# Performance work log

Hardware: AMD Instinct MI355X
Metric: run time of the kernel (lower is better)

## Reference

```python
import jax, jax.numpy as jnp
import numpy as np

DIM = 384
EPS = 1e-12  # F.normalize default eps


def setup_inputs() -> dict:
    key = jax.random.key(0)
    ks = jax.random.split(key, 6)
    b, c, h, w = 4, DIM, 64, 64
    x = jax.random.normal(ks[0], (b, c, h, w), dtype=jnp.float32)
    gamma = jnp.ones((c,), dtype=jnp.float32)  # WanRMS_norm gamma, init ones
    # 1x1 convs are per-pixel linear maps: [out_c, in_c] weight + bias
    w_qkv = jax.random.normal(ks[1], (3 * c, c), dtype=jnp.float32) * (1.0 / np.sqrt(c))
    b_qkv = jax.random.normal(ks[2], (3 * c,), dtype=jnp.float32) * 0.01
    w_proj = jax.random.normal(ks[3], (c, c), dtype=jnp.float32) * (1.0 / np.sqrt(c))
    b_proj = jax.random.normal(ks[4], (c,), dtype=jnp.float32) * 0.01
    return {"x": x, "gamma": gamma, "w_qkv": w_qkv, "b_qkv": b_qkv,
            "w_proj": w_proj, "b_proj": b_proj}


def reference(x, gamma, w_qkv, b_qkv, w_proj, b_proj):
    b, c, h, w = x.shape
    identity = x
    # WanRMS_norm: F.normalize over channel dim * sqrt(dim) * gamma
    l2 = jnp.sqrt(jnp.sum(x * x, axis=1, keepdims=True))
    xn = x / jnp.maximum(l2, EPS) * jnp.sqrt(jnp.float32(c)) * gamma[None, :, None, None]
    # 1x1 conv qkv: [b, 3c, h, w]
    qkv = jnp.einsum("bchw,oc->bohw", xn, w_qkv) + b_qkv[None, :, None, None]
    # flatten spatial -> tokens: [b, 3c, s] -> q/k/v each [b, s, c]
    s = h * w
    qkv = qkv.reshape(b, 3 * c, s).transpose(0, 2, 1)  # [b, s, 3c]
    q, k, v = jnp.split(qkv, 3, axis=-1)
    # single-head scaled dot-product attention (non-causal, as in Wan SDPA call)
    scores = jnp.einsum("bqc,bkc->bqk", q, k) / jnp.sqrt(jnp.float32(c))
    attn = jax.nn.softmax(scores, axis=-1)
    out = jnp.einsum("bqk,bkc->bqc", attn, v)  # [b, s, c]
    out = out.transpose(0, 2, 1).reshape(b, c, h, w)
    # 1x1 proj conv + residual
    out = jnp.einsum("bchw,oc->bohw", out, w_proj) + b_proj[None, :, None, None]
    return out + identity
```

## Files before the change

kernel.cpp:

```cpp
#include <hip/hip_runtime.h>
#include <cstdint>
#include <cstddef>

typedef __bf16 bf16;
typedef __bf16 bf16x8 __attribute__((ext_vector_type(8)));
typedef float  f32x4 __attribute__((ext_vector_type(4)));
typedef float  f32x16 __attribute__((ext_vector_type(16)));
typedef int    i32x4 __attribute__((ext_vector_type(4)));
typedef int    i32x8 __attribute__((ext_vector_type(8)));

#define MFMA16(a, b, c) __builtin_amdgcn_mfma_f32_16x16x32_bf16((a), (b), (c), 0, 0, 0)
#define MFMA_MX(a, b, c) \
    __builtin_amdgcn_mfma_scale_f32_32x32x64_f8f6f4((a), (b), (c), 0, 0, 0, 0x7F, 0, 0x7F)

__device__ __forceinline__ uint8_t to_fp8(float v) {
    return (uint8_t)(__builtin_amdgcn_cvt_pk_fp8_f32(v, v, 0, false) & 0xff);
}

__device__ __forceinline__ i32x8 ld32(const void* p) {
    i32x4 a = *(const i32x4*)p;
    i32x4 b = *(const i32x4*)((const char*)p + 16);
    i32x8 r;
    r[0] = a[0]; r[1] = a[1]; r[2] = a[2]; r[3] = a[3];
    r[4] = b[0]; r[5] = b[1]; r[6] = b[2]; r[7] = b[3];
    return r;
}

__device__ __forceinline__ void gload16(const void* g, void* l) {
    __builtin_amdgcn_global_load_lds(
        (const __attribute__((address_space(1))) unsigned int*)g,
        (__attribute__((address_space(3))) unsigned int*)l,
        16, 0, 0);
}

__global__ __launch_bounds__(256) void convert_w(
    const float* __restrict__ wqkv, const float* __restrict__ wproj,
    bf16* __restrict__ wq, bf16* __restrict__ wp)
{
    int t = blockIdx.x * 256 + threadIdx.x;
    if (t < 1152 * 384) wq[t] = (bf16)wqkv[t];
    else                wp[t - 1152 * 384] = (bf16)wproj[t - 1152 * 384];
}

__global__ __launch_bounds__(64) void norm_kernel(
    const float* __restrict__ x, const float* __restrict__ gamma,
    bf16* __restrict__ xn)
{
    __shared__ float sG[384];
    int tid = threadIdx.x;
    for (int i = tid; i < 384; i += 64) sG[i] = gamma[i];
    __syncthreads();
    int t = blockIdx.x * 64 + tid;
    int b = t >> 12, p = t & 4095;
    const float* xb = x + (size_t)(b * 384) * 4096 + p;
    float ss = 0.f;
    for (int c = 0; c < 384; ++c) { float v = xb[(size_t)c * 4096]; ss += v * v; }
    float scale = 19.595917942265423f / fmaxf(sqrtf(ss), 1e-12f);
    bf16* o = xn + (size_t)t * 384;
    for (int c0 = 0; c0 < 384; c0 += 8) {
        bf16x8 v8;
#pragma unroll
        for (int j = 0; j < 8; ++j)
            v8[j] = (bf16)(xb[(size_t)(c0 + j) * 4096] * scale * sG[c0 + j]);
        *(bf16x8*)(o + c0) = v8;
    }
}

__global__ __launch_bounds__(256) void gemm_bt(
    const bf16* __restrict__ A, const bf16* __restrict__ B,
    const float* __restrict__ bias_m, const float* __restrict__ bias_n,
    const float* __restrict__ resid, void* __restrict__ Cout,
    int mode, int ldc)
{
    __shared__ bf16 sA[128 * 72];
    __shared__ bf16 sB[128 * 72];
    const int tid = threadIdx.x;
    const int l = tid & 63, w = tid >> 6;
    const int lo = l & 15, hi = l >> 4;
    const int wm = w >> 1, wn = w & 1;
    const int m0 = blockIdx.y * 128, n0 = blockIdx.x * 128;

    f32x4 acc[4][4] = {};

    for (int kt = 0; kt < 6; ++kt) {
        __syncthreads();
        const int k0 = kt * 64;
#pragma unroll
        for (int i = 0; i < 5; ++i) {
            int ci = i * 256 + tid;
            if (ci < 1152) {
                int row = ci / 9, off = ci % 9;
                gload16(A + (size_t)(m0 + row) * 384 + k0 + off * 8, (char*)sA + ci * 16);
                gload16(B + (size_t)(n0 + row) * 384 + k0 + off * 8, (char*)sB + ci * 16);
            }
        }
        __syncthreads();
#pragma unroll
        for (int ks = 0; ks < 2; ++ks) {
            bf16x8 af[4], bfr[4];
#pragma unroll
            for (int t = 0; t < 4; ++t)
                af[t] = *(const bf16x8*)(sA + (wm * 64 + t * 16 + lo) * 72 + ks * 32 + hi * 8);
#pragma unroll
            for (int t = 0; t < 4; ++t)
                bfr[t] = *(const bf16x8*)(sB + (wn * 64 + t * 16 + lo) * 72 + ks * 32 + hi * 8);
#pragma unroll
            for (int rt = 0; rt < 4; ++rt)
#pragma unroll
                for (int ct = 0; ct < 4; ++ct)
                    acc[rt][ct] = MFMA16(af[rt], bfr[ct], acc[rt][ct]);
        }
    }

#pragma unroll
    for (int rt = 0; rt < 4; ++rt) {
#pragma unroll
        for (int ct = 0; ct < 4; ++ct) {
            int mb = m0 + wm * 64 + rt * 16 + hi * 4;
            int n  = n0 + wn * 64 + ct * 16 + lo;
            if (mode == 0) {
                uint8_t* C = (uint8_t*)Cout;
                float bn = bias_n[n];
#pragma unroll
                for (int r = 0; r < 4; ++r)
                    C[(size_t)(mb + r) * ldc + n] = to_fp8(acc[rt][ct][r] + bn);
            } else if (mode == 1) {
                uint8_t* C = (uint8_t*)Cout;
#pragma unroll
                for (int r = 0; r < 4; ++r)
                    C[(size_t)(mb + r) * ldc + n] = to_fp8(acc[rt][ct][r] + bias_m[mb + r]);
            } else {
                float* O = (float*)Cout;
                int bb = n >> 12, p = n & 4095;
#pragma unroll
                for (int r = 0; r < 4; ++r) {
                    int m = mb + r;
                    size_t idx = ((size_t)(bb * 384 + m)) * 4096 + p;
                    O[idx] = acc[rt][ct][r] + bias_m[m] + resid[idx];
                }
            }
        }
    }
}

__device__ __forceinline__ void stage_tiles64(
    const uint8_t* __restrict__ qk, const uint8_t* __restrict__ vt,
    int kv0, uint8_t* sK, uint8_t* sV, int tid)
{
    const uint8_t* kb = qk + (size_t)kv0 * 768 + 384;
#pragma unroll
    for (int i = 0; i < 7; ++i) {
        int ci = i * 256 + tid;
        if (ci < 1600) {
            int row = ci / 25, off = ci % 25;
            gload16(kb + (size_t)row * 768 + off * 16, sK + ci * 16);
        }
    }
    const uint8_t* vb = vt + kv0;
#pragma unroll
    for (int i = 0; i < 8; ++i) {
        int ci = i * 256 + tid;
        if (ci < 1920) {
            int row = ci / 5, off = ci % 5;
            gload16(vb + (size_t)row * 16384 + off * 16, sV + ci * 16);
        }
    }
}

__global__ __launch_bounds__(256, 2) void flash_kernel(
    const uint8_t* __restrict__ qk, const uint8_t* __restrict__ vt,
    bf16* __restrict__ op0, bf16* __restrict__ op1, float* __restrict__ ml)
{
    __shared__ char smem[56320];
    uint8_t* sK = (uint8_t*)smem;
    uint8_t* sV = (uint8_t*)smem + 25600;
    const int tid = threadIdx.x;
    const int l = tid & 63, w = tid >> 6;
    const int l31 = l & 31, hi2 = l >> 5;
    const int wq = w >> 1, wd = w & 1;
    const int qt = blockIdx.x, bh = blockIdx.y;
    const int b = bh >> 1, half = bh & 1;
    const int q0 = b * 4096 + qt * 64;
    const int kvbase = b * 4096 + half * 2048;
    const float SC = 0.07362217057594547f;

    i32x8 qf[6];
    {
        const uint8_t* qrow = qk + (size_t)(q0 + wq * 32 + l31) * 768 + hi2 * 32;
#pragma unroll
        for (int ksw = 0; ksw < 6; ++ksw)
            qf[ksw] = ld32(qrow + ksw * 64);
    }

    f32x16 o[6] = {};
    float m = -1e30f, lsum = 0.f;

    for (int kt = 0; kt < 32; ++kt) {
        stage_tiles64(qk, vt, kvbase + kt * 64, sK, sV, tid);
        __syncthreads();

        f32x16 s0 = {}, s1 = {};
#pragma unroll
        for (int ksw = 0; ksw < 6; ++ksw) {
            i32x8 ak0 = ld32(sK + (size_t)l31 * 400 + ksw * 64 + hi2 * 32);
            i32x8 ak1 = ld32(sK + (size_t)(32 + l31) * 400 + ksw * 64 + hi2 * 32);
            s0 = MFMA_MX(ak0, qf[ksw], s0);
            s1 = MFMA_MX(ak1, qf[ksw], s1);
        }

        float mx = s0[0];
#pragma unroll
        for (int r = 1; r < 16; ++r) mx = fmaxf(mx, s0[r]);
#pragma unroll
        for (int r = 0; r < 16; ++r) mx = fmaxf(mx, s1[r]);
        mx = fmaxf(mx, __shfl_xor(mx, 32));
        if (__any(mx > m)) {
            float mn = fmaxf(m, mx);
            float alpha = exp2f((m - mn) * SC);
            m = mn;
            lsum *= alpha;
#pragma unroll
            for (int dt = 0; dt < 6; ++dt)
#pragma unroll
                for (int r = 0; r < 16; ++r) o[dt][r] *= alpha;
        }
        float p0[16], p1[16];
        float rs = 0.f;
        float msc = m * SC;
#pragma unroll
        for (int r = 0; r < 16; ++r) { p0[r] = exp2f(fmaf(s0[r], SC, -msc)); rs += p0[r]; }
#pragma unroll
        for (int r = 0; r < 16; ++r) { p1[r] = exp2f(fmaf(s1[r], SC, -msc)); rs += p1[r]; }
        rs += __shfl_xor(rs, 32);
        lsum += rs;

        int pk0[4], pk1[4];
#pragma unroll
        for (int i = 0; i < 4; ++i) {
            int d = __builtin_amdgcn_cvt_pk_fp8_f32(p0[4 * i], p0[4 * i + 1], 0, false);
            pk0[i] = __builtin_amdgcn_cvt_pk_fp8_f32(p0[4 * i + 2], p0[4 * i + 3], d, true);
            d = __builtin_amdgcn_cvt_pk_fp8_f32(p1[4 * i], p1[4 * i + 1], 0, false);
            pk1[i] = __builtin_amdgcn_cvt_pk_fp8_f32(p1[4 * i + 2], p1[4 * i + 3], d, true);
        }
        i32x8 pf;
#pragma unroll
        for (int i = 0; i < 4; ++i) {
            int x0 = __shfl_xor(pk0[i], 32);
            int x1 = __shfl_xor(pk1[i], 32);
            int own = hi2 ? pk1[i] : pk0[i];
            int oth = hi2 ? x1 : x0;
            pf[2 * i]     = hi2 ? oth : own;
            pf[2 * i + 1] = hi2 ? own : oth;
        }

#pragma unroll
        for (int dt = 0; dt < 6; ++dt) {
            i32x8 av = ld32(sV + (size_t)(wd * 192 + dt * 32 + l31) * 80 + hi2 * 32);
            o[dt] = MFMA_MX(av, pf, o[dt]);
        }

        __syncthreads();
    }

    float* tr = (float*)(smem + w * 4608);
    bf16* dst = half ? op1 : op0;
#pragma unroll
    for (int dt = 0; dt < 6; ++dt) {
#pragma unroll
        for (int r = 0; r < 16; ++r) {
            int d32 = (r & 3) + 8 * (r >> 2) + 4 * hi2;
            tr[l31 * 36 + d32] = o[dt][r];
        }
        f32x4 v0 = *(f32x4*)(tr + l31 * 36 + hi2 * 16 + 0);
        f32x4 v1 = *(f32x4*)(tr + l31 * 36 + hi2 * 16 + 4);
        f32x4 v2 = *(f32x4*)(tr + l31 * 36 + hi2 * 16 + 8);
        f32x4 v3 = *(f32x4*)(tr + l31 * 36 + hi2 * 16 + 12);
        bf16x8 h0, h1;
#pragma unroll
        for (int j = 0; j < 4; ++j) {
            h0[j] = (bf16)v0[j]; h0[4 + j] = (bf16)v1[j];
            h1[j] = (bf16)v2[j]; h1[4 + j] = (bf16)v3[j];
        }
        size_t tok = (size_t)(q0 + wq * 32 + l31);
        bf16* drow = dst + tok * 384 + wd * 192 + dt * 32 + hi2 * 16;
        *(bf16x8*)(drow + 0) = h0;
        *(bf16x8*)(drow + 8) = h1;
        __syncthreads();
    }
    if (wd == 0 && hi2 == 0) {
        int tok = q0 + wq * 32 + l31;
        ml[(size_t)(half * 16384 + tok) * 2 + 0] = m * SC;
        ml[(size_t)(half * 16384 + tok) * 2 + 1] = lsum;
    }
}

__global__ __launch_bounds__(256) void merge_kernel(
    const bf16* __restrict__ p0, const bf16* __restrict__ p1,
    const float* __restrict__ ml, bf16* __restrict__ ob)
{
    int tok = blockIdx.x * 4 + (threadIdx.x >> 6);
    int l = threadIdx.x & 63;
    float m0 = ml[(size_t)tok * 2 + 0], l0 = ml[(size_t)tok * 2 + 1];
    float m1 = ml[(size_t)(16384 + tok) * 2 + 0], l1 = ml[(size_t)(16384 + tok) * 2 + 1];
    float mM = fmaxf(m0, m1);
    float a0 = exp2f(m0 - mM), a1 = exp2f(m1 - mM);
    float inv = 1.0f / (a0 * l0 + a1 * l1);
    float w0 = a0 * inv, w1 = a1 * inv;
    if (l < 48) {
        size_t off = (size_t)tok * 384 + l * 8;
        bf16x8 v0 = *(const bf16x8*)(p0 + off);
        bf16x8 v1 = *(const bf16x8*)(p1 + off);
        bf16x8 r;
#pragma unroll
        for (int j = 0; j < 8; ++j)
            r[j] = (bf16)((float)v0[j] * w0 + (float)v1[j] * w1);
        *(bf16x8*)(ob + off) = r;
    }
}

extern "C" void kernel_launch(void* const* d_in, const int* in_sizes, int n_in,
                              void* d_out, int out_size, void* d_ws, size_t ws_size,
                              hipStream_t stream) {
    const float* x      = (const float*)d_in[0];
    const float* gamma  = (const float*)d_in[1];
    const float* w_qkv  = (const float*)d_in[2];
    const float* b_qkv  = (const float*)d_in[3];
    const float* w_proj = (const float*)d_in[4];
    const float* b_proj = (const float*)d_in[5];
    float* out = (float*)d_out;

    char* ws = (char*)d_ws;
    bf16* xn  = (bf16*)ws;    ws += (size_t)16384 * 384 * 2;
    uint8_t* qkb = (uint8_t*)ws; ws += (size_t)16384 * 768;
    uint8_t* vtb = (uint8_t*)ws; ws += (size_t)384 * 16384;
    bf16* ob  = (bf16*)ws;    ws += (size_t)16384 * 384 * 2;
    bf16* wq  = (bf16*)ws;    ws += (size_t)1152 * 384 * 2;
    bf16* wp  = (bf16*)ws;    ws += (size_t)384 * 384 * 2;
    float* mlb = (float*)ws;  ws += (size_t)2 * 16384 * 2 * 4;

    convert_w<<<2304, 256, 0, stream>>>(w_qkv, w_proj, wq, wp);
    norm_kernel<<<256, 64, 0, stream>>>(x, gamma, xn);
    gemm_bt<<<dim3(6, 128), 256, 0, stream>>>(xn, wq, nullptr, b_qkv, nullptr, qkb, 0, 768);
    gemm_bt<<<dim3(128, 3), 256, 0, stream>>>(wq + (size_t)768 * 384, xn,
                                              b_qkv + 768, nullptr, nullptr, vtb, 1, 16384);
    flash_kernel<<<dim3(64, 8), 256, 0, stream>>>(qkb, vtb, xn, ob, mlb);
    merge_kernel<<<4096, 256, 0, stream>>>(xn, ob, mlb, ob);
    gemm_bt<<<dim3(128, 3), 256, 0, stream>>>(wp, ob, b_proj, nullptr, x, out, 2, 0);
}
```

Measured before the change: 288.6 us.

## Double-buffer LDS tiles in GEMM and flash attention with raw barriers

The GEMM kernel now double-buffers its A/B LDS tiles, prefetching the next k-slice while the current one is consumed. It uses explicit vmcnt waits and raw s_barrier instead of paired __syncthreads. The flash kernel splits K and V staging: K is double-buffered and prefetched one tile ahead, while V is loaded at the start of each iteration and awaited with a partial vmcnt only before the PV MFMAs. This overlaps global-to-LDS copies with the QK and softmax compute. The cost is larger LDS footprints and a hand-counted vmcnt that depends on the exact number of loads each thread issues.

After: 292.9 us. Within noise of the previous version (+1.5%).

```diff
diff --git a/kernel.cpp b/kernel.cpp
--- a/kernel.cpp
+++ b/kernel.cpp
@@ -12,6 +12,9 @@
 #define MFMA16(a, b, c) __builtin_amdgcn_mfma_f32_16x16x32_bf16((a), (b), (c), 0, 0, 0)
 #define MFMA_MX(a, b, c) \
     __builtin_amdgcn_mfma_scale_f32_32x32x64_f8f6f4((a), (b), (c), 0, 0, 0, 0x7F, 0, 0x7F)
+
+#define WAIT_VM(N) asm volatile("s_waitcnt vmcnt(" #N ")" ::: "memory")
+#define RAW_BARRIER() __builtin_amdgcn_s_barrier()
 
 __device__ __forceinline__ uint8_t to_fp8(float v) {
     return (uint8_t)(__builtin_amdgcn_cvt_pk_fp8_f32(v, v, 0, false) & 0xff);
@@ -66,14 +69,28 @@
     }
 }
 
-__global__ __launch_bounds__(256) void gemm_bt(
+__device__ __forceinline__ void gemm_stage(
+    const bf16* __restrict__ A, const bf16* __restrict__ B,
+    int m0, int n0, int k0, bf16* sA, bf16* sB, int tid)
+{
+#pragma unroll
+    for (int i = 0; i < 5; ++i) {
+        int ci = i * 256 + tid;
+        if (ci < 1152) {
+            int row = ci / 9, off = ci % 9;
+            gload16(A + (size_t)(m0 + row) * 384 + k0 + off * 8, (char*)sA + ci * 16);
+            gload16(B + (size_t)(n0 + row) * 384 + k0 + off * 8, (char*)sB + ci * 16);
+        }
+    }
+}
+
+__global__ __launch_bounds__(256, 2) void gemm_bt(
     const bf16* __restrict__ A, const bf16* __restrict__ B,
     const float* __restrict__ bias_m, const float* __restrict__ bias_n,
     const float* __restrict__ resid, void* __restrict__ Cout,
     int mode, int ldc)
 {
-    __shared__ bf16 sA[128 * 72];
-    __shared__ bf16 sB[128 * 72];
+    __shared__ char smem[73728];
     const int tid = threadIdx.x;
     const int l = tid & 63, w = tid >> 6;
     const int lo = l & 15, hi = l >> 4;
@@ -82,19 +99,17 @@
 
     f32x4 acc[4][4] = {};
 
+    gemm_stage(A, B, m0, n0, 0, (bf16*)smem, (bf16*)(smem + 36864), tid);
+
     for (int kt = 0; kt < 6; ++kt) {
-        __syncthreads();
-        const int k0 = kt * 64;
-#pragma unroll
-        for (int i = 0; i < 5; ++i) {
-            int ci = i * 256 + tid;
-            if (ci < 1152) {
-                int row = ci / 9, off = ci % 9;
-                gload16(A + (size_t)(m0 + row) * 384 + k0 + off * 8, (char*)sA + ci * 16);
-                gload16(B + (size_t)(n0 + row) * 384 + k0 + off * 8, (char*)sB + ci * 16);
-            }
-        }
-        __syncthreads();
+        WAIT_VM(0);
+        RAW_BARRIER();
+        if (kt < 5)
+            gemm_stage(A, B, m0, n0, (kt + 1) * 64,
+                       (bf16*)(smem + ((kt + 1) & 1) * 18432),
+                       (bf16*)(smem + 36864 + ((kt + 1) & 1) * 18432), tid);
+        const bf16* sA = (const bf16*)(smem + (kt & 1) * 18432);
+        const bf16* sB = (const bf16*)(smem + 36864 + (kt & 1) * 18432);
 #pragma unroll
         for (int ks = 0; ks < 2; ++ks) {
             bf16x8 af[4], bfr[4];
@@ -143,9 +158,8 @@
     }
 }
 
-__device__ __forceinline__ void stage_tiles64(
-    const uint8_t* __restrict__ qk, const uint8_t* __restrict__ vt,
-    int kv0, uint8_t* sK, uint8_t* sV, int tid)
+__device__ __forceinline__ void stage_K64(
+    const uint8_t* __restrict__ qk, int kv0, uint8_t* sK, int tid)
 {
     const uint8_t* kb = qk + (size_t)kv0 * 768 + 384;
 #pragma unroll
@@ -156,6 +170,10 @@
             gload16(kb + (size_t)row * 768 + off * 16, sK + ci * 16);
         }
     }
+}
+__device__ __forceinline__ void stage_V64(
+    const uint8_t* __restrict__ vt, int kv0, uint8_t* sV, int tid)
+{
     const uint8_t* vb = vt + kv0;
 #pragma unroll
     for (int i = 0; i < 8; ++i) {
@@ -171,9 +189,7 @@
     const uint8_t* __restrict__ qk, const uint8_t* __restrict__ vt,
     bf16* __restrict__ op0, bf16* __restrict__ op1, float* __restrict__ ml)
 {
-    __shared__ char smem[56320];
-    uint8_t* sK = (uint8_t*)smem;
-    uint8_t* sV = (uint8_t*)smem + 25600;
+    __shared__ char smem[81920];
     const int tid = threadIdx.x;
     const int l = tid & 63, w = tid >> 6;
     const int l31 = l & 31, hi2 = l >> 5;
@@ -183,6 +199,7 @@
     const int q0 = b * 4096 + qt * 64;
     const int kvbase = b * 4096 + half * 2048;
     const float SC = 0.07362217057594547f;
+    uint8_t* sV = (uint8_t*)smem + 51200;
 
     i32x8 qf[6];
     {
@@ -195,9 +212,15 @@
     f32x16 o[6] = {};
     float m = -1e30f, lsum = 0.f;
 
+    stage_K64(qk, kvbase, (uint8_t*)smem, tid);
+
     for (int kt = 0; kt < 32; ++kt) {
-        stage_tiles64(qk, vt, kvbase + kt * 64, sK, sV, tid);
-        __syncthreads();
+        WAIT_VM(0);
+        RAW_BARRIER();
+        stage_V64(vt, kvbase + kt * 64, sV, tid);
+        if (kt < 31)
+            stage_K64(qk, kvbase + (kt + 1) * 64, (uint8_t*)smem + ((kt + 1) & 1) * 25600, tid);
+        const uint8_t* sK = (const uint8_t*)smem + (kt & 1) * 25600;
 
         f32x16 s0 = {}, s1 = {};
 #pragma unroll
@@ -253,14 +276,16 @@
             pf[2 * i + 1] = hi2 ? own : oth;
         }
 
+        if (kt < 31) WAIT_VM(6); else WAIT_VM(0);
+        RAW_BARRIER();
+
 #pragma unroll
         for (int dt = 0; dt < 6; ++dt) {
             i32x8 av = ld32(sV + (size_t)(wd * 192 + dt * 32 + l31) * 80 + hi2 * 32);
             o[dt] = MFMA_MX(av, pf, o[dt]);
         }
-
-        __syncthreads();
-    }
+    }
+    __syncthreads();
 
     float* tr = (float*)(smem + w * 4608);
     bf16* dst = half ? op1 : op0;
```
